# Performance work log

Measured on AMD Instinct MI355X. Metric: run time of the kernel, lower is better.

Reference implementation:

```python
import jax, jax.numpy as jnp
import numpy as np

N = 40000      # nodes
E = 640000     # edges
G = 64         # graphs in batch
F_IN = 128
H = 128


def setup_inputs() -> dict:
    key = jax.random.key(0)
    ks = jax.random.split(key, 10)
    x = jax.random.normal(ks[0], (N, F_IN), dtype=jnp.float32)
    edge_index = jax.random.randint(ks[1], (2, E), 0, N, dtype=jnp.int64)
    batch = jnp.sort(jax.random.randint(ks[2], (N,), 0, G, dtype=jnp.int64))
    s = 0.05
    W1 = jax.random.normal(ks[3], (F_IN, H), dtype=jnp.float32) * s
    W2 = jax.random.normal(ks[4], (H, H), dtype=jnp.float32) * s
    W3 = jax.random.normal(ks[5], (H, H), dtype=jnp.float32) * s
    Wl = jax.random.normal(ks[6], (H, 1), dtype=jnp.float32) * s
    b1 = jnp.zeros((H,), jnp.float32)
    b2 = jnp.zeros((H,), jnp.float32)
    b3 = jnp.zeros((H,), jnp.float32)
    bl = jnp.zeros((1,), jnp.float32)
    return {"x": x, "edge_index": edge_index, "batch": batch, "dropout_rate": 0,
            "W1": W1, "b1": b1, "W2": W2, "b2": b2, "W3": W3, "b3": b3,
            "Wl": Wl, "bl": bl}


def _gcn_norm(edge_index, n):
    # PyG GCNConv default: add self-loops, symmetric deg^{-1/2} normalization.
    loop = jnp.arange(n, dtype=edge_index.dtype)
    row = jnp.concatenate([edge_index[0], loop])  # source
    col = jnp.concatenate([edge_index[1], loop])  # target
    ones = jnp.ones(row.shape[0], jnp.float32)
    deg = jax.ops.segment_sum(ones, col, num_segments=n)
    dis = jnp.where(deg > 0, jax.lax.rsqrt(deg), 0.0)
    norm = dis[row] * dis[col]  # [E+N]
    return row, col, norm


def _gcn_conv(x, row, col, norm, W, b, n):
    h = x @ W + b                       # dense transform [N,H]
    msg = h[row] * norm[:, None]        # gather + scale  [E+N,H]
    return jax.ops.segment_sum(msg, col, num_segments=n)


def reference(x, edge_index, batch, dropout_rate, W1, b1, W2, b2, W3, b3, Wl, bl):
    n = x.shape[0]
    row, col, norm = _gcn_norm(edge_index, n)
    # eval mode: dropout(p=dropout_rate, training=False) is identity
    h = jax.nn.relu(_gcn_conv(x, row, col, norm, W1, b1, n))
    h = jax.nn.relu(_gcn_conv(h, row, col, norm, W2, b2, n))
    h = jax.nn.relu(_gcn_conv(h, row, col, norm, W3, b3, n))
    # global mean pool over graphs
    sums = jax.ops.segment_sum(h, batch, num_segments=G)           # [G,H]
    cnt = jax.ops.segment_sum(jnp.ones(n, jnp.float32), batch, num_segments=G)
    pooled = sums / jnp.maximum(cnt, 1.0)[:, None]
    return pooled @ Wl + bl             # [G,1]
```

## Files before the change

kernel.cpp:

```cpp
#include <hip/hip_runtime.h>

constexpr int N = 40000;
constexpr int E = 640000;
constexpr int G = 64;
constexpr int H = 128;

constexpr int NB      = (N + 255) / 256;
constexpr int EB      = (E + 255) / 256;
constexpr int GEMM1_B = N / 64;
constexpr int FUSED_B = N / 32;
constexpr int POOL_B  = N / 32;

constexpr int CAP     = 64;
constexpr int QPN     = CAP / 4;
constexpr int CSRE    = N * CAP + 8;
constexpr int STAMP_B = (N * QPN + 255) / 256;

typedef float    floatx2 __attribute__((ext_vector_type(2)));
typedef float    f32x4   __attribute__((ext_vector_type(4)));
typedef _Float16 f16x8   __attribute__((ext_vector_type(8)));

__device__ __forceinline__ unsigned pack_fp8x4(float a, float b, float c, float d) {
    unsigned v = 0;
    v = __builtin_amdgcn_cvt_pk_fp8_f32(a, b, v, false);
    v = __builtin_amdgcn_cvt_pk_fp8_f32(c, d, v, true);
    return v;
}

__device__ __forceinline__ void pk_fma(floatx2& acc, floatx2 a, floatx2 w2) {
    asm("v_pk_fma_f32 %0, %1, %2, %0" : "+v"(acc) : "v"(a), "v"(w2));
}

__device__ __forceinline__ void fma8p(floatx2& aclo, floatx2& achi, unsigned r, float w) {
    floatx2 lo = __builtin_amdgcn_cvt_pk_f32_fp8(r, false);
    floatx2 hi = __builtin_amdgcn_cvt_pk_f32_fp8(r, true);
    floatx2 w2 = {w, w};
    pk_fma(aclo, lo, w2);
    pk_fma(achi, hi, w2);
}

__device__ __forceinline__ float entry_w(int e) {
    floatx2 hi = __builtin_amdgcn_cvt_pk_f32_fp8((unsigned)e, true);
    return hi.y;
}
__device__ __forceinline__ int entry_src(int e) { return e & 0xFFFFFF; }

__device__ __forceinline__ f16x8 cvt8(float4 a, float4 b) {
    f16x8 r;
    r[0] = (_Float16)a.x; r[1] = (_Float16)a.y; r[2] = (_Float16)a.z; r[3] = (_Float16)a.w;
    r[4] = (_Float16)b.x; r[5] = (_Float16)b.y; r[6] = (_Float16)b.z; r[7] = (_Float16)b.w;
    return r;
}

__device__ __forceinline__ float4 aggregate_node(const unsigned* __restrict__ h8,
                                                 const int4* __restrict__ csr4,
                                                 const int* __restrict__ cnt,
                                                 const float* __restrict__ dis,
                                                 int i, int c) {
    float d = dis[i];
    floatx2 aclo = {0.f, 0.f}, achi = {0.f, 0.f};
    fma8p(aclo, achi, h8[(size_t)i * 32 + c], d * d);
    int cq = cnt[i]; cq = (cq > CAP) ? CAP : cq;
    int p  = i * QPN;
    int p1 = p + (((cq + 7) & ~7) >> 2);
    for (; p < p1; p += 2) {
        int4 ea = csr4[p], eb = csr4[p + 1];
        unsigned r0 = h8[(size_t)entry_src(ea.x) * 32 + c];
        unsigned r1 = h8[(size_t)entry_src(ea.y) * 32 + c];
        unsigned r2 = h8[(size_t)entry_src(ea.z) * 32 + c];
        unsigned r3 = h8[(size_t)entry_src(ea.w) * 32 + c];
        unsigned r4 = h8[(size_t)entry_src(eb.x) * 32 + c];
        unsigned r5 = h8[(size_t)entry_src(eb.y) * 32 + c];
        unsigned r6 = h8[(size_t)entry_src(eb.z) * 32 + c];
        unsigned r7 = h8[(size_t)entry_src(eb.w) * 32 + c];
        fma8p(aclo, achi, r0, entry_w(ea.x)); fma8p(aclo, achi, r1, entry_w(ea.y));
        fma8p(aclo, achi, r2, entry_w(ea.z)); fma8p(aclo, achi, r3, entry_w(ea.w));
        fma8p(aclo, achi, r4, entry_w(eb.x)); fma8p(aclo, achi, r5, entry_w(eb.y));
        fma8p(aclo, achi, r6, entry_w(eb.z)); fma8p(aclo, achi, r7, entry_w(eb.w));
    }
    return make_float4(aclo.x, aclo.y, achi.x, achi.y);
}

__global__ void prep_wt1(const float* __restrict__ W1, _Float16* __restrict__ wt) {
    const int g  = blockIdx.x * 256 + threadIdx.x;
    const int f  = g >> 4;
    const int k0 = (g & 15) * 8;
    f16x8 v;
    #pragma unroll
    for (int j = 0; j < 8; ++j) v[j] = (_Float16)W1[(size_t)(k0 + j) * H + f];
    *reinterpret_cast<f16x8*>(wt + f * H + k0) = v;
}

__global__ __launch_bounds__(256) void gemm1_and_fill(const float* __restrict__ X,
                                                      const _Float16* __restrict__ wt1,
                                                      const float* __restrict__ b,
                                                      unsigned* __restrict__ Y,
                                                      const int* __restrict__ row,
                                                      const int* __restrict__ col,
                                                      int* __restrict__ cursor,
                                                      int* __restrict__ csr,
                                                      const float* __restrict__ W2,
                                                      const float* __restrict__ W3,
                                                      _Float16* __restrict__ wt) {
    __shared__ uint4 WTl[2048];
    const int blk = blockIdx.x;
    const int tid = threadIdx.x;
    if (blk >= GEMM1_B + EB) {
        const int pb = blk - (GEMM1_B + EB);
        const int m  = 1 + (pb >> 3);
        const float* W = (m == 1) ? W2 : W3;
        const int g  = (pb & 7) * 256 + tid;
        const int f  = g >> 4;
        const int k0 = (g & 15) * 8;
        f16x8 v;
        #pragma unroll
        for (int j = 0; j < 8; ++j) v[j] = (_Float16)W[(size_t)(k0 + j) * H + f];
        *reinterpret_cast<f16x8*>(wt + ((size_t)m << 14) + f * H + k0) = v;
        return;
    }
    if (blk >= GEMM1_B) {
        int e = (blk - GEMM1_B) * 256 + tid;
        if (e < E) {
            int rsrc = row[e], cdst = col[e];
            int p = atomicAdd(&cursor[cdst], 1);
            if (p < CAP) csr[cdst * CAP + p] = rsrc + 1;
        }
        return;
    }
    const uint4* wtg = reinterpret_cast<const uint4*>(wt1);
    #pragma unroll
    for (int i = 0; i < 8; ++i) {
        int g = i * 256 + tid;
        WTl[g ^ ((g >> 4) & 7)] = wtg[g];
    }
    __syncthreads();

    const int lane = tid & 63;
    const int wv   = tid >> 6;
    const int c    = lane & 15;
    const int grp  = lane >> 4;
    const int node = blk * 64 + wv * 16 + c;

    const f32x4* b4 = reinterpret_cast<const f32x4*>(b);
    f32x4 acc[8];
    #pragma unroll
    for (int mt = 0; mt < 8; ++mt) acc[mt] = b4[mt * 4 + grp];

    const float4* X4 = reinterpret_cast<const float4*>(X);
    #pragma unroll
    for (int ks = 0; ks < 4; ++ks) {
        const int k0 = ks * 32 + grp * 8;
        float4 xa = X4[(size_t)node * 32 + (k0 >> 2)];
        float4 xb = X4[(size_t)node * 32 + (k0 >> 2) + 1];
        f16x8 bfr = cvt8(xa, xb);
        #pragma unroll
        for (int mt = 0; mt < 8; ++mt) {
            const int f = mt * 16 + c;
            const int g = (f << 4) + (k0 >> 3);
            f16x8 afr = *reinterpret_cast<const f16x8*>(&WTl[g ^ (f & 7)]);
            acc[mt] = __builtin_amdgcn_mfma_f32_16x16x32_f16(afr, bfr, acc[mt], 0, 0, 0);
        }
    }
    #pragma unroll
    for (int mt = 0; mt < 8; ++mt) {
        const int jg = mt * 4 + grp;
        Y[(size_t)node * 32 + jg] = pack_fp8x4(acc[mt][0], acc[mt][1], acc[mt][2], acc[mt][3]);
    }
}

__global__ __launch_bounds__(256) void stamp_weights(int* __restrict__ csr,
                                                     const int* __restrict__ cursor,
                                                     float* __restrict__ dis) {
    const int q = blockIdx.x * 256 + threadIdx.x;
    const int node = q >> 4;
    const int qi   = q & 15;
    if (node >= N) return;
    const int cd = cursor[node];
    const float rd = rsqrtf((float)(cd + 1));
    if (qi == 0) dis[node] = rd;
    int cq = (cd > CAP) ? CAP : cd;
    const int padq = ((cq + 7) & ~7) >> 2;
    if (qi >= padq) return;
    int4* csr4 = reinterpret_cast<int4*>(csr);
    int4 e = csr4[q];
    auto st = [&](int v) -> int {
        if (v == 0) return 0;
        int src = v - 1;
        float w = rsqrtf((float)(cursor[src] + 1)) * rd;
        unsigned wb = __builtin_amdgcn_cvt_pk_fp8_f32(w, 0.0f, 0, false) & 0xFFu;
        return (int)((wb << 24) | (unsigned)src);
    };
    e.x = st(e.x); e.y = st(e.y); e.z = st(e.z); e.w = st(e.w);
    csr4[q] = e;
}

__global__ __launch_bounds__(256) void fused_agg_gemm(const unsigned* __restrict__ t_in,
                                                      const int4* __restrict__ csr4,
                                                      const int* __restrict__ cnt,
                                                      const float* __restrict__ dis,
                                                      const _Float16* __restrict__ wt,
                                                      const float* __restrict__ b,
                                                      unsigned* __restrict__ t_out) {
    __shared__ float4 tile[32 * 32];
    const int tid = threadIdx.x;
    const int node0 = blockIdx.x * 32;

    {
        const int cc = tid & 31;
        const int nl = tid >> 5;
        #pragma unroll
        for (int sub = 0; sub < 4; ++sub) {
            const int local = sub * 8 + nl;
            float4 acc = aggregate_node(t_in, csr4, cnt, dis, node0 + local, cc);
            acc.x = fmaxf(acc.x, 0.f); acc.y = fmaxf(acc.y, 0.f);
            acc.z = fmaxf(acc.z, 0.f); acc.w = fmaxf(acc.w, 0.f);
            tile[(local * 32 + cc) ^ (local & 7)] = acc;
        }
    }
    __syncthreads();

    const int lane = tid & 63;
    const int wv   = tid >> 6;
    const int c    = lane & 15;
    const int grp  = lane >> 4;

    const f32x4* b4 = reinterpret_cast<const f32x4*>(b);
    f32x4 acc00, acc01, acc10, acc11;
    acc00 = acc01 = b4[(2 * wv + 0) * 4 + grp];
    acc10 = acc11 = b4[(2 * wv + 1) * 4 + grp];

    const uint4* wtg = reinterpret_cast<const uint4*>(wt);
    #pragma unroll
    for (int ks = 0; ks < 4; ++ks) {
        const int k0 = ks * 32 + grp * 8;
        f16x8 bfr0, bfr1;
        {
            int nd = c;
            int g0 = nd * 32 + (k0 >> 2);
            float4 ta = tile[g0 ^ (nd & 7)];
            float4 tb = tile[(g0 + 1) ^ (nd & 7)];
            bfr0 = cvt8(ta, tb);
            nd = 16 + c;
            g0 = nd * 32 + (k0 >> 2);
            ta = tile[g0 ^ (nd & 7)];
            tb = tile[(g0 + 1) ^ (nd & 7)];
            bfr1 = cvt8(ta, tb);
        }
        {
            int f = (2 * wv + 0) * 16 + c;
            f16x8 afr = *reinterpret_cast<const f16x8*>(&wtg[f * 16 + (k0 >> 3)]);
            acc00 = __builtin_amdgcn_mfma_f32_16x16x32_f16(afr, bfr0, acc00, 0, 0, 0);
            acc01 = __builtin_amdgcn_mfma_f32_16x16x32_f16(afr, bfr1, acc01, 0, 0, 0);
            f = (2 * wv + 1) * 16 + c;
            afr = *reinterpret_cast<const f16x8*>(&wtg[f * 16 + (k0 >> 3)]);
            acc10 = __builtin_amdgcn_mfma_f32_16x16x32_f16(afr, bfr0, acc10, 0, 0, 0);
            acc11 = __builtin_amdgcn_mfma_f32_16x16x32_f16(afr, bfr1, acc11, 0, 0, 0);
        }
    }

    const int jg0 = (2 * wv + 0) * 4 + grp;
    const int jg1 = (2 * wv + 1) * 4 + grp;
    const int nA = node0 + c, nB = node0 + 16 + c;
    t_out[(size_t)nA * 32 + jg0] = pack_fp8x4(acc00[0], acc00[1], acc00[2], acc00[3]);
    t_out[(size_t)nB * 32 + jg0] = pack_fp8x4(acc01[0], acc01[1], acc01[2], acc01[3]);
    t_out[(size_t)nA * 32 + jg1] = pack_fp8x4(acc10[0], acc10[1], acc10[2], acc10[3]);
    t_out[(size_t)nB * 32 + jg1] = pack_fp8x4(acc11[0], acc11[1], acc11[2], acc11[3]);
}

__global__ __launch_bounds__(256) void agg_pool(const unsigned* __restrict__ t_in,
                                                const int4* __restrict__ csr4,
                                                const int* __restrict__ cnt,
                                                const float* __restrict__ dis,
                                                const int* __restrict__ batch,
                                                float* __restrict__ pooled) {
    __shared__ float4 tile[32 * 32];
    const int tid = threadIdx.x;
    const int c  = tid & 31;
    const int nl = tid >> 5;
    const int i0 = blockIdx.x * 32;

    #pragma unroll
    for (int sub = 0; sub < 4; ++sub) {
        const int local = sub * 8 + nl;
        float4 acc = aggregate_node(t_in, csr4, cnt, dis, i0 + local, c);
        acc.x = fmaxf(acc.x, 0.f); acc.y = fmaxf(acc.y, 0.f);
        acc.z = fmaxf(acc.z, 0.f); acc.w = fmaxf(acc.w, 0.f);
        tile[local * 32 + c] = acc;
    }
    __syncthreads();

    if (tid < 128) {
        const int j = tid;
        const float* tf = reinterpret_cast<const float*>(tile);
        int cur = batch[i0];
        float s = 0.0f;
        #pragma unroll
        for (int r = 0; r < 32; ++r) {
            int g = batch[i0 + r];
            if (g != cur) { atomicAdd(&pooled[cur * H + j], s); s = 0.0f; cur = g; }
            s += tf[r * 128 + j];
        }
        atomicAdd(&pooled[cur * H + j], s);
    }
}

__global__ __launch_bounds__(128) void head(const float* __restrict__ pooled,
                                            const int* __restrict__ batch,
                                            const float* __restrict__ Wl,
                                            const float* __restrict__ bl,
                                            float* __restrict__ out) {
    const int g = blockIdx.x;
    const int j = threadIdx.x;
    __shared__ int bounds[2];
    if (j < 2) {
        int target = g + j;
        int lo = 0, hi = N;
        while (lo < hi) {
            int mid = (lo + hi) >> 1;
            if (batch[mid] < target) lo = mid + 1; else hi = mid;
        }
        bounds[j] = lo;
    }
    __syncthreads();
    float cnt = fmaxf((float)(bounds[1] - bounds[0]), 1.0f);
    float val = (pooled[g * H + j] / cnt) * Wl[j];
    __shared__ float red[128];
    red[j] = val;
    __syncthreads();
    #pragma unroll
    for (int s = 64; s > 0; s >>= 1) {
        if (j < s) red[j] += red[j + s];
        __syncthreads();
    }
    if (j == 0) out[g] = red[0] + bl[0];
}

extern "C" void kernel_launch(void* const* d_in, const int* in_sizes, int n_in,
                              void* d_out, int out_size, void* d_ws, size_t ws_size,
                              hipStream_t stream) {
    const float* x     = (const float*)d_in[0];
    const int*   ei    = (const int*)  d_in[1];
    const int*   batch = (const int*)  d_in[2];
    const float* W1 = (const float*)d_in[4];
    const float* b1 = (const float*)d_in[5];
    const float* W2 = (const float*)d_in[6];
    const float* b2 = (const float*)d_in[7];
    const float* W3 = (const float*)d_in[8];
    const float* b3 = (const float*)d_in[9];
    const float* Wl = (const float*)d_in[10];
    const float* bl = (const float*)d_in[11];
    float* out = (float*)d_out;

    const int* row = ei;
    const int* col = ei + E;

    auto align256 = [](size_t v) { return (v + 255) & ~(size_t)255; };
    char* ws = (char*)d_ws;
    size_t off = 0;
    int*   cursor = (int*)(ws + off);
    float* pooled = (float*)(cursor + N);
    int*   csr    = (int*)(pooled + (size_t)G * H);
    size_t zero_bytes = (size_t)N * 4 + (size_t)G * H * 4 + (size_t)CSRE * 4;
    off += align256(zero_bytes);
    float*    dis = (float*)(ws + off); off += align256((size_t)N * 4);
    _Float16* wt  = (_Float16*)(ws + off); off += align256((size_t)3 * H * H * 2);
    unsigned* bufA = (unsigned*)(ws + off); off += align256((size_t)N * H);
    unsigned* bufB = (unsigned*)(ws + off); off += align256((size_t)N * H);
    (void)ws_size; (void)n_in; (void)in_sizes; (void)out_size;

    const int4* csr4 = reinterpret_cast<const int4*>(csr);
    _Float16* wt1 = wt;
    _Float16* wt2 = wt + (size_t)H * H;
    _Float16* wt3 = wt + (size_t)2 * H * H;

    (void)hipMemsetAsync(cursor, 0, zero_bytes, stream);
    prep_wt1<<<8, 256, 0, stream>>>(W1, wt1);
    gemm1_and_fill<<<GEMM1_B + EB + 16, 256, 0, stream>>>(x, wt1, b1, bufA, row, col,
                                                          cursor, csr, W2, W3, wt);
    stamp_weights<<<STAMP_B, 256, 0, stream>>>(csr, cursor, dis);
    fused_agg_gemm<<<FUSED_B, 256, 0, stream>>>(bufA, csr4, cursor, dis, wt2, b2, bufB);
    fused_agg_gemm<<<FUSED_B, 256, 0, stream>>>(bufB, csr4, cursor, dis, wt3, b3, bufA);
    agg_pool<<<POOL_B, 256, 0, stream>>>(bufA, csr4, cursor, dis, batch, pooled);
    head<<<G, 128, 0, stream>>>(pooled, batch, Wl, bl, out);
}
```

Measured before the change: 215.8 us.

## Split CSR build into count, prefix, and stamped fill with per-XCD counters

```diff
diff --git a/kernel.cpp b/kernel.cpp
--- a/kernel.cpp
+++ b/kernel.cpp
@@ -10,11 +10,11 @@
 constexpr int GEMM1_B = N / 64;
 constexpr int FUSED_B = N / 32;
 constexpr int POOL_B  = N / 32;
+constexpr int NXCD    = 8;
 
 constexpr int CAP     = 64;
 constexpr int QPN     = CAP / 4;
 constexpr int CSRE    = N * CAP + 8;
-constexpr int STAMP_B = (N * QPN + 255) / 256;
 
 typedef float    floatx2 __attribute__((ext_vector_type(2)));
 typedef float    f32x4   __attribute__((ext_vector_type(4)));
@@ -54,13 +54,13 @@
 
 __device__ __forceinline__ float4 aggregate_node(const unsigned* __restrict__ h8,
                                                  const int4* __restrict__ csr4,
-                                                 const int* __restrict__ cnt,
+                                                 const int* __restrict__ deg,
                                                  const float* __restrict__ dis,
                                                  int i, int c) {
     float d = dis[i];
     floatx2 aclo = {0.f, 0.f}, achi = {0.f, 0.f};
     fma8p(aclo, achi, h8[(size_t)i * 32 + c], d * d);
-    int cq = cnt[i]; cq = (cq > CAP) ? CAP : cq;
+    int cq = deg[i]; cq = (cq > CAP) ? CAP : cq;
     int p  = i * QPN;
     int p1 = p + (((cq + 7) & ~7) >> 2);
     for (; p < p1; p += 2) {
@@ -91,17 +91,15 @@
     *reinterpret_cast<f16x8*>(wt + f * H + k0) = v;
 }
 
-__global__ __launch_bounds__(256) void gemm1_and_fill(const float* __restrict__ X,
-                                                      const _Float16* __restrict__ wt1,
-                                                      const float* __restrict__ b,
-                                                      unsigned* __restrict__ Y,
-                                                      const int* __restrict__ row,
-                                                      const int* __restrict__ col,
-                                                      int* __restrict__ cursor,
-                                                      int* __restrict__ csr,
-                                                      const float* __restrict__ W2,
-                                                      const float* __restrict__ W3,
-                                                      _Float16* __restrict__ wt) {
+__global__ __launch_bounds__(256) void gemm1_and_count8(const float* __restrict__ X,
+                                                        const _Float16* __restrict__ wt1,
+                                                        const float* __restrict__ b,
+                                                        unsigned* __restrict__ Y,
+                                                        const int* __restrict__ col,
+                                                        int* __restrict__ cnt8,
+                                                        const float* __restrict__ W2,
+                                                        const float* __restrict__ W3,
+                                                        _Float16* __restrict__ wt) {
     __shared__ uint4 WTl[2048];
     const int blk = blockIdx.x;
     const int tid = threadIdx.x;
@@ -121,9 +119,8 @@
     if (blk >= GEMM1_B) {
         int e = (blk - GEMM1_B) * 256 + tid;
         if (e < E) {
-            int rsrc = row[e], cdst = col[e];
-            int p = atomicAdd(&cursor[cdst], 1);
-            if (p < CAP) csr[cdst * CAP + p] = rsrc + 1;
+            int r = (e >> 8) & 7;
+            atomicAdd(&cnt8[r * N + col[e]], 1);
         }
         return;
     }
@@ -168,35 +165,39 @@
     }
 }
 
-__global__ __launch_bounds__(256) void stamp_weights(int* __restrict__ csr,
-                                                     const int* __restrict__ cursor,
-                                                     float* __restrict__ dis) {
-    const int q = blockIdx.x * 256 + threadIdx.x;
-    const int node = q >> 4;
-    const int qi   = q & 15;
-    if (node >= N) return;
-    const int cd = cursor[node];
-    const float rd = rsqrtf((float)(cd + 1));
-    if (qi == 0) dis[node] = rd;
-    int cq = (cd > CAP) ? CAP : cd;
-    const int padq = ((cq + 7) & ~7) >> 2;
-    if (qi >= padq) return;
-    int4* csr4 = reinterpret_cast<int4*>(csr);
-    int4 e = csr4[q];
-    auto st = [&](int v) -> int {
-        if (v == 0) return 0;
-        int src = v - 1;
-        float w = rsqrtf((float)(cursor[src] + 1)) * rd;
-        unsigned wb = __builtin_amdgcn_cvt_pk_fp8_f32(w, 0.0f, 0, false) & 0xFFu;
-        return (int)((wb << 24) | (unsigned)src);
-    };
-    e.x = st(e.x); e.y = st(e.y); e.z = st(e.z); e.w = st(e.w);
-    csr4[q] = e;
+__global__ void mid_deg_dis(int* __restrict__ cnt8, int* __restrict__ deg,
+                            float* __restrict__ dis) {
+    int i = blockIdx.x * 256 + threadIdx.x;
+    if (i >= N) return;
+    int base = 0;
+    #pragma unroll
+    for (int r = 0; r < NXCD; ++r) {
+        int v = cnt8[r * N + i];
+        cnt8[r * N + i] = base;
+        base += v;
+    }
+    deg[i] = base;
+    dis[i] = rsqrtf((float)(base + 1));
+}
+
+__global__ __launch_bounds__(256) void fill_stamped(const int* __restrict__ row,
+                                                    const int* __restrict__ col,
+                                                    const float* __restrict__ dis,
+                                                    int* __restrict__ cnt8,
+                                                    int* __restrict__ csr) {
+    int e = blockIdx.x * 256 + threadIdx.x;
+    if (e >= E) return;
+    int rsrc = row[e], cdst = col[e];
+    float w = dis[rsrc] * dis[cdst];
+    unsigned wb = __builtin_amdgcn_cvt_pk_fp8_f32(w, 0.0f, 0, false) & 0xFFu;
+    int r = (e >> 8) & 7;
+    int p = atomicAdd(&cnt8[r * N + cdst], 1);
+    if (p < CAP) csr[cdst * CAP + p] = (int)((wb << 24) | (unsigned)rsrc);
 }
 
 __global__ __launch_bounds__(256) void fused_agg_gemm(const unsigned* __restrict__ t_in,
                                                       const int4* __restrict__ csr4,
-                                                      const int* __restrict__ cnt,
+                                                      const int* __restrict__ deg,
                                                       const float* __restrict__ dis,
                                                       const _Float16* __restrict__ wt,
                                                       const float* __restrict__ b,
@@ -211,7 +212,7 @@
         #pragma unroll
         for (int sub = 0; sub < 4; ++sub) {
             const int local = sub * 8 + nl;
-            float4 acc = aggregate_node(t_in, csr4, cnt, dis, node0 + local, cc);
+            float4 acc = aggregate_node(t_in, csr4, deg, dis, node0 + local, cc);
             acc.x = fmaxf(acc.x, 0.f); acc.y = fmaxf(acc.y, 0.f);
             acc.z = fmaxf(acc.z, 0.f); acc.w = fmaxf(acc.w, 0.f);
             tile[(local * 32 + cc) ^ (local & 7)] = acc;
@@ -269,7 +270,7 @@
 
 __global__ __launch_bounds__(256) void agg_pool(const unsigned* __restrict__ t_in,
                                                 const int4* __restrict__ csr4,
-                                                const int* __restrict__ cnt,
+                                                const int* __restrict__ deg,
                                                 const float* __restrict__ dis,
                                                 const int* __restrict__ batch,
                                                 float* __restrict__ pooled) {
@@ -282,7 +283,7 @@
     #pragma unroll
     for (int sub = 0; sub < 4; ++sub) {
         const int local = sub * 8 + nl;
-        float4 acc = aggregate_node(t_in, csr4, cnt, dis, i0 + local, c);
+        float4 acc = aggregate_node(t_in, csr4, deg, dis, i0 + local, c);
         acc.x = fmaxf(acc.x, 0.f); acc.y = fmaxf(acc.y, 0.f);
         acc.z = fmaxf(acc.z, 0.f); acc.w = fmaxf(acc.w, 0.f);
         tile[local * 32 + c] = acc;
@@ -357,12 +358,13 @@
     auto align256 = [](size_t v) { return (v + 255) & ~(size_t)255; };
     char* ws = (char*)d_ws;
     size_t off = 0;
-    int*   cursor = (int*)(ws + off);
-    float* pooled = (float*)(cursor + N);
+    int*   cnt8   = (int*)(ws + off);
+    float* pooled = (float*)(cnt8 + (size_t)NXCD * N);
     int*   csr    = (int*)(pooled + (size_t)G * H);
-    size_t zero_bytes = (size_t)N * 4 + (size_t)G * H * 4 + (size_t)CSRE * 4;
+    size_t zero_bytes = (size_t)NXCD * N * 4 + (size_t)G * H * 4 + (size_t)CSRE * 4;
     off += align256(zero_bytes);
     float*    dis = (float*)(ws + off); off += align256((size_t)N * 4);
+    int*      deg = (int*)  (ws + off); off += align256((size_t)N * 4);
     _Float16* wt  = (_Float16*)(ws + off); off += align256((size_t)3 * H * H * 2);
     unsigned* bufA = (unsigned*)(ws + off); off += align256((size_t)N * H);
     unsigned* bufB = (unsigned*)(ws + off); off += align256((size_t)N * H);
@@ -373,13 +375,14 @@
     _Float16* wt2 = wt + (size_t)H * H;
     _Float16* wt3 = wt + (size_t)2 * H * H;
 
-    (void)hipMemsetAsync(cursor, 0, zero_bytes, stream);
+    (void)hipMemsetAsync(cnt8, 0, zero_bytes, stream);
     prep_wt1<<<8, 256, 0, stream>>>(W1, wt1);
-    gemm1_and_fill<<<GEMM1_B + EB + 16, 256, 0, stream>>>(x, wt1, b1, bufA, row, col,
-                                                          cursor, csr, W2, W3, wt);
-    stamp_weights<<<STAMP_B, 256, 0, stream>>>(csr, cursor, dis);
-    fused_agg_gemm<<<FUSED_B, 256, 0, stream>>>(bufA, csr4, cursor, dis, wt2, b2, bufB);
-    fused_agg_gemm<<<FUSED_B, 256, 0, stream>>>(bufB, csr4, cursor, dis, wt3, b3, bufA);
-    agg_pool<<<POOL_B, 256, 0, stream>>>(bufA, csr4, cursor, dis, batch, pooled);
+    gemm1_and_count8<<<GEMM1_B + EB + 16, 256, 0, stream>>>(x, wt1, b1, bufA, col,
+                                                            cnt8, W2, W3, wt);
+    mid_deg_dis<<<NB, 256, 0, stream>>>(cnt8, deg, dis);
+    fill_stamped<<<EB, 256, 0, stream>>>(row, col, dis, cnt8, csr);
+    fused_agg_gemm<<<FUSED_B, 256, 0, stream>>>(bufA, csr4, deg, dis, wt2, b2, bufB);
+    fused_agg_gemm<<<FUSED_B, 256, 0, stream>>>(bufB, csr4, deg, dis, wt3, b3, bufA);
+    agg_pool<<<POOL_B, 256, 0, stream>>>(bufA, csr4, deg, dis, batch, pooled);
     head<<<G, 128, 0, stream>>>(pooled, batch, Wl, bl, out);
 }
```

Result: no change. 218.7 us (+1.3%).
